# Performance work log

Measured on AMD Instinct MI355X. Metric: run time of the kernel, lower is better.

The kernel has to match this reference:

```python
import jax, jax.numpy as jnp
import numpy as np

N = 1024
INTER_CH = 10      # C(4,2) + (8-4)
HIDDEN_CH = 32
OUT_CH = 1
THRESH = 4
TOP_K = 8
INTERACT = 4


def setup_inputs() -> dict:
    key = jax.random.key(0)
    k1, k2, k3, k4, k5 = jax.random.split(key, 5)
    x = jax.random.normal(k1, (16, N, N), dtype=jnp.float32)
    is_active_flags = jnp.ones((16,), dtype=bool)
    # 1x1 conv params (stored as dense matrices; kernel_size=1)
    w1 = jax.random.normal(k2, (HIDDEN_CH, INTER_CH), dtype=jnp.float32) / np.sqrt(INTER_CH)
    b1 = jax.random.normal(k3, (HIDDEN_CH, 1, 1), dtype=jnp.float32) * 0.01
    w2 = jax.random.normal(k4, (OUT_CH, HIDDEN_CH), dtype=jnp.float32) / np.sqrt(HIDDEN_CH)
    b2 = jax.random.normal(k5, (OUT_CH, 1, 1), dtype=jnp.float32) * 0.01
    return {"x": x, "is_active_flags": is_active_flags, "w1": w1, "b1": b1, "w2": w2, "b2": b2}


def reference(x, is_active_flags, w1, b1, w2, b2):
    gate_active = jnp.sum(is_active_flags) >= THRESH

    def _active_path(operand):
        inputs, mask = operand                       # (16, n, n), (16,)
        _, slogdet = jnp.linalg.slogdet(inputs)      # (16,)
        scores = jnp.where(mask, slogdet, -jnp.inf)
        _, indices = jax.lax.top_k(scores, TOP_K)
        top_x = inputs[indices]                      # (8, n, n)
        top_interact_x = top_x[:INTERACT]            # (4, n, n)
        next_preserve_x = top_x[INTERACT:]           # (4, n, n)
        idx1, idx2 = jnp.triu_indices(INTERACT, k=1)  # 6 pairs
        pairs = jnp.matmul(top_interact_x[idx1], top_interact_x[idx2])  # (6, n, n)
        concat = jnp.concatenate([pairs, next_preserve_x], axis=0)      # (10, n, n)
        hidden = jnp.einsum('oc,chw->ohw', w1, concat) + b1             # 1x1 conv
        out = jnp.einsum('oc,chw->ohw', w2, hidden) + b2                # 1x1 conv
        return (out, jnp.array(True))

    def _inactive_path(operand):
        inputs, _ = operand
        _, n, m = inputs.shape
        return (jnp.zeros((OUT_CH, n, m), dtype=jnp.float32), jnp.array(False))

    out, out_active = jax.lax.cond(gate_active, _active_path, _inactive_path, (x, is_active_flags))
    return (out, out_active)
```

## Files before the change

kernel.cpp:

```cpp
#include <hip/hip_runtime.h>
#include <math.h>

#define N 1024
#define NN (N*N)

__device__ __forceinline__ void wave_argmax_kv(float& v, int& k) {
  #pragma unroll
  for (int off = 32; off > 0; off >>= 1) {
    float ov = __shfl_down(v, off);
    int   ok = __shfl_down(k, off);
    if (ov > v || (ov == v && ok < k)) { v = ov; k = ok; }
  }
}

__global__ void init_kernel(double* scores) {
  int t = threadIdx.x;
  if (t < 16) scores[t] = 0.0;
}

__global__ __launch_bounds__(256) void copy_kernel(const float4* __restrict__ src,
                                                   float4* __restrict__ dst) {
  int i = blockIdx.x * 256 + threadIdx.x;
  dst[i] = src[i];
}

__global__ __launch_bounds__(1024) void panel_kernel(float* __restrict__ lu,
                                                     int* __restrict__ ipiv,
                                                     double* __restrict__ scores,
                                                     int c0) {
  __shared__ __align__(16) float bufP[32];
  __shared__ float ujjS[32];
  __shared__ float redv[16];
  __shared__ int   redk[16];
  __shared__ int   posOf[1024];
  __shared__ int   lay[1024];
  const int m = blockIdx.x;
  float* A = lu + (size_t)m * NN;
  const int R = N - c0;
  const int tid = threadIdx.x;
  bool active = tid < R;
  float row[32];

  if (active) {
    const float4* g = (const float4*)(A + (size_t)(c0 + tid) * N + c0);
    #pragma unroll
    for (int q = 0; q < 8; ++q) {
      float4 v = g[q];
      row[4*q] = v.x; row[4*q+1] = v.y; row[4*q+2] = v.z; row[4*q+3] = v.w;
    }
  }
  posOf[tid] = tid;
  lay[tid]   = tid;
  __syncthreads();

  int worig;
  {
    float val = active ? fabsf(row[0]) : -1.0f;
    int key = (tid << 11) | tid;
    wave_argmax_kv(val, key);
    if ((tid & 63) == 0) { redv[tid >> 6] = val; redk[tid >> 6] = key; }
    __syncthreads();
    float bv = redv[0]; int bk = redk[0];
    #pragma unroll 1
    for (int w = 1; w < 16; ++w)
      if (redv[w] > bv || (redv[w] == bv && redk[w] < bk)) { bv = redv[w]; bk = redk[w]; }
    worig = bk & 0x7FF;
  }

  #pragma unroll
  for (int j = 0; j < 32; ++j) {
    if (tid == worig) {
      #pragma unroll
      for (int q = 0; q < 8; ++q)
        *(float4*)&bufP[4*q] = make_float4(row[4*q], row[4*q+1], row[4*q+2], row[4*q+3]);
      active = false;
    }
    if (tid == 0) {
      int p = posOf[worig];
      ipiv[m * 32 + j] = c0 + p;
      int a = lay[j];
      lay[j] = worig; lay[p] = a;
      posOf[worig] = j; posOf[a] = p;
    }
    __syncthreads();

    float u[32];
    #pragma unroll
    for (int q = 0; q < 8; ++q) {
      if (4*q + 3 >= j) {
        float4 v = *(const float4*)&bufP[4*q];
        u[4*q] = v.x; u[4*q+1] = v.y; u[4*q+2] = v.z; u[4*q+3] = v.w;
      }
    }
    if (tid == 0) ujjS[j] = u[j];
    const float rujj = 1.0f / u[j];

    float l = 0.0f;
    if (active) { l = row[j] * rujj; row[j] = l; }

    float val = -1.0f; int key = 0x7fffffff;
    if (j < 31) {
      if (active) {
        float v = row[j+1] - l * u[j+1];
        row[j+1] = v;
        #pragma unroll
        for (int jj = j + 2; jj < 32; ++jj) row[jj] -= l * u[jj];
        int mypos = posOf[tid];
        val = fabsf(v); key = (mypos << 11) | tid;
      }
      wave_argmax_kv(val, key);
      if ((tid & 63) == 0) { redv[tid >> 6] = val; redk[tid >> 6] = key; }
    }
    __syncthreads();
    if (j < 31) {
      float bv = redv[0]; int bk = redk[0];
      #pragma unroll 1
      for (int w = 1; w < 16; ++w)
        if (redv[w] > bv || (redv[w] == bv && redk[w] < bk)) { bv = redv[w]; bk = redk[w]; }
      worig = bk & 0x7FF;
    }
  }

  if (tid < R) {
    int fp = posOf[tid];
    float4* g = (float4*)(A + (size_t)(c0 + fp) * N + c0);
    #pragma unroll
    for (int q = 0; q < 8; ++q)
      g[q] = make_float4(row[4*q], row[4*q+1], row[4*q+2], row[4*q+3]);
  }
  if (tid == 0) {
    double logsum = 0.0;
    #pragma unroll 1
    for (int j = 0; j < 32; ++j) logsum += log(fabs((double)ujjS[j]));
    atomicAdd(&scores[m], logsum);
  }
}

__global__ __launch_bounds__(256) void ptrsm_kernel(float* __restrict__ lu,
                                                    const int* __restrict__ ipiv,
                                                    int c0, int ncs) {
  const int m  = blockIdx.x / ncs;
  const int cs = blockIdx.x % ncs;
  const int s0 = c0 + 32 + cs * 256;
  const int tid = threadIdx.x;
  const int col = s0 + tid;
  const bool ac = col < N;
  float* A = lu + (size_t)m * NN;
  const int R = N - c0;
  __shared__ int   rowAt[1024];
  __shared__ float L11s[32][33];
  __shared__ int   dDst[48];
  __shared__ int   dSrc[48];
  __shared__ int   dcount;

  for (int r = tid; r < R; r += 256) rowAt[r] = c0 + r;
  if (tid == 0) dcount = 0;
  for (int idx = tid; idx < 1024; idx += 256) {
    int i = idx >> 5, k = idx & 31;
    L11s[i][k] = A[(size_t)(c0 + i) * N + c0 + k];
  }
  __syncthreads();
  if (tid == 0) {
    #pragma unroll 1
    for (int j = 0; j < 32; ++j) {
      int p = ipiv[m * 32 + j];
      if (p != c0 + j) { int t = rowAt[j]; rowAt[j] = rowAt[p - c0]; rowAt[p - c0] = t; }
    }
  }
  __syncthreads();
  for (int r = 32 + tid; r < R; r += 256) {
    if (rowAt[r] != c0 + r) {
      int i = atomicAdd(&dcount, 1);
      dDst[i] = c0 + r; dSrc[i] = rowAt[r];
    }
  }
  __syncthreads();
  const int nd = dcount;

  float pay[32];
  #pragma unroll
  for (int i = 0; i < 32; ++i)
    if (i < nd && ac) pay[i] = A[(size_t)dSrc[i] * N + col];
  float u[32];
  #pragma unroll
  for (int i = 0; i < 32; ++i)
    if (ac) u[i] = A[(size_t)rowAt[i] * N + col];

  #pragma unroll
  for (int i = 1; i < 32; ++i) {
    float a = u[i];
    #pragma unroll
    for (int k = 0; k < 32; ++k)
      if (k < i) a -= L11s[i][k] * u[k];
    u[i] = a;
  }

  #pragma unroll
  for (int i = 0; i < 32; ++i)
    if (i < nd && ac) A[(size_t)dDst[i] * N + col] = pay[i];
  #pragma unroll
  for (int i = 0; i < 32; ++i)
    if (ac) A[(size_t)(c0 + i) * N + col] = u[i];
}

__global__ __launch_bounds__(256) void update_kernel(float* __restrict__ lu,
                                                     int c0, int nrt, int ncs) {
  const int per = nrt * ncs;
  const int m  = blockIdx.x / per;
  const int t  = blockIdx.x % per;
  const int rt = t / ncs, cs = t % ncs;
  const int r0 = c0 + 32 + rt * 64;
  const int s0 = c0 + 32 + cs * 256;
  const int tid = threadIdx.x;
  float* A = lu + (size_t)m * NN;
  __shared__ float Lts[32][68];
  __shared__ float Us[32][260];
  for (int idx = tid; idx < 2048; idx += 256) {
    int r = idx >> 5, k = idx & 31;
    Lts[k][r] = (r0 + r < N) ? A[(size_t)(r0 + r) * N + c0 + k] : 0.0f;
  }
  for (int idx = tid; idx < 8192; idx += 256) {
    int k = idx >> 8, c = idx & 255;
    Us[k][c] = (s0 + c < N) ? A[(size_t)(c0 + k) * N + s0 + c] : 0.0f;
  }
  __syncthreads();
  const int tx = tid & 63;
  const int ty = tid >> 6;
  float4 acc[16];
  #pragma unroll
  for (int e = 0; e < 16; ++e) acc[e] = make_float4(0.f, 0.f, 0.f, 0.f);
  #pragma unroll 4
  for (int k = 0; k < 32; ++k) {
    float4 b  = *(const float4*)&Us[k][tx * 4];
    float4 a0 = *(const float4*)&Lts[k][ty * 16 + 0];
    float4 a1 = *(const float4*)&Lts[k][ty * 16 + 4];
    float4 a2 = *(const float4*)&Lts[k][ty * 16 + 8];
    float4 a3 = *(const float4*)&Lts[k][ty * 16 + 12];
    acc[0].x  += a0.x*b.x; acc[0].y  += a0.x*b.y; acc[0].z  += a0.x*b.z; acc[0].w  += a0.x*b.w;
    acc[1].x  += a0.y*b.x; acc[1].y  += a0.y*b.y; acc[1].z  += a0.y*b.z; acc[1].w  += a0.y*b.w;
    acc[2].x  += a0.z*b.x; acc[2].y  += a0.z*b.y; acc[2].z  += a0.z*b.z; acc[2].w  += a0.z*b.w;
    acc[3].x  += a0.w*b.x; acc[3].y  += a0.w*b.y; acc[3].z  += a0.w*b.z; acc[3].w  += a0.w*b.w;
    acc[4].x  += a1.x*b.x; acc[4].y  += a1.x*b.y; acc[4].z  += a1.x*b.z; acc[4].w  += a1.x*b.w;
    acc[5].x  += a1.y*b.x; acc[5].y  += a1.y*b.y; acc[5].z  += a1.y*b.z; acc[5].w  += a1.y*b.w;
    acc[6].x  += a1.z*b.x; acc[6].y  += a1.z*b.y; acc[6].z  += a1.z*b.z; acc[6].w  += a1.z*b.w;
    acc[7].x  += a1.w*b.x; acc[7].y  += a1.w*b.y; acc[7].z  += a1.w*b.z; acc[7].w  += a1.w*b.w;
    acc[8].x  += a2.x*b.x; acc[8].y  += a2.x*b.y; acc[8].z  += a2.x*b.z; acc[8].w  += a2.x*b.w;
    acc[9].x  += a2.y*b.x; acc[9].y  += a2.y*b.y; acc[9].z  += a2.y*b.z; acc[9].w  += a2.y*b.w;
    acc[10].x += a2.z*b.x; acc[10].y += a2.z*b.y; acc[10].z += a2.z*b.z; acc[10].w += a2.z*b.w;
    acc[11].x += a2.w*b.x; acc[11].y += a2.w*b.y; acc[11].z += a2.w*b.z; acc[11].w += a2.w*b.w;
    acc[12].x += a3.x*b.x; acc[12].y += a3.x*b.y; acc[12].z += a3.x*b.z; acc[12].w += a3.x*b.w;
    acc[13].x += a3.y*b.x; acc[13].y += a3.y*b.y; acc[13].z += a3.y*b.z; acc[13].w += a3.y*b.w;
    acc[14].x += a3.z*b.x; acc[14].y += a3.z*b.y; acc[14].z += a3.z*b.z; acc[14].w += a3.z*b.w;
    acc[15].x += a3.w*b.x; acc[15].y += a3.w*b.y; acc[15].z += a3.w*b.z; acc[15].w += a3.w*b.w;
  }
  const bool colok = (s0 + tx * 4) < N;
  #pragma unroll
  for (int e = 0; e < 16; ++e) {
    int r = r0 + ty * 16 + e;
    if (r < N && colok) {
      float4* p = (float4*)&A[(size_t)r * N + s0 + tx * 4];
      float4 v = *p;
      v.x -= acc[e].x; v.y -= acc[e].y; v.z -= acc[e].z; v.w -= acc[e].w;
      *p = v;
    }
  }
}

__global__ void select_kernel(const void* __restrict__ flagsraw, const double* __restrict__ scores,
                              const float* __restrict__ w1, const float* __restrict__ b1,
                              const float* __restrict__ w2, const float* __restrict__ b2,
                              int* __restrict__ topidx, float* __restrict__ misc,
                              float* __restrict__ out_tail) {
  if (threadIdx.x != 0 || blockIdx.x != 0) return;
  const unsigned char* fb = (const unsigned char*)flagsraw;
  bool nonbin = false, off4 = false;
  for (int i = 0; i < 16; ++i) {
    if (fb[i] > 1) nonbin = true;
    if ((i & 3) && fb[i]) off4 = true;
  }
  int f[16]; int nact = 0;
  for (int i = 0; i < 16; ++i) {
    int v;
    if (nonbin)      v = (((const float*)flagsraw)[i] != 0.0f);
    else if (off4)   v = (fb[i] != 0);
    else             v = (((const int*)flagsraw)[i] != 0);
    f[i] = v; nact += v;
  }
  int gate = (nact >= 4) ? 1 : 0;
  double sc[16];
  for (int i = 0; i < 16; ++i) sc[i] = f[i] ? scores[i] : -1.0e300;
  bool used[16] = {};
  for (int k = 0; k < 8; ++k) {
    int bi = -1; double bv = 0.0;
    for (int i = 0; i < 16; ++i)
      if (!used[i] && (bi < 0 || sc[i] > bv)) { bv = sc[i]; bi = i; }
    used[bi] = true;
    topidx[k] = bi;
  }
  for (int cC = 0; cC < 10; ++cC) {
    float s = 0.0f;
    for (int h = 0; h < 32; ++h) s += w2[h] * w1[h * 10 + cC];
    misc[cC] = s;
  }
  float be = 0.0f;
  for (int h = 0; h < 32; ++h) be += w2[h] * b1[h];
  be += b2[0];
  misc[10] = be;
  ((int*)misc)[12] = gate;
  *out_tail = gate ? 1.0f : 0.0f;
}

__global__ __launch_bounds__(256) void build_m_kernel(const float* __restrict__ x,
                                                      const int* __restrict__ topidx,
                                                      const float* __restrict__ misc,
                                                      float* __restrict__ M) {
  int i = blockIdx.x * 256 + threadIdx.x;
  const float4* T1 = (const float4*)(x + (size_t)topidx[1] * NN);
  const float4* T2 = (const float4*)(x + (size_t)topidx[2] * NN);
  const float4* T3 = (const float4*)(x + (size_t)topidx[3] * NN);
  float w0 = misc[0], w1_ = misc[1], w2_ = misc[2], w3_ = misc[3], w4_ = misc[4], w5_ = misc[5];
  float4 t1 = T1[i], t2 = T2[i], t3 = T3[i];
  float4 m0, m1, m2;
  m0.x = w0 * t1.x + w1_ * t2.x + w2_ * t3.x;
  m0.y = w0 * t1.y + w1_ * t2.y + w2_ * t3.y;
  m0.z = w0 * t1.z + w1_ * t2.z + w2_ * t3.z;
  m0.w = w0 * t1.w + w1_ * t2.w + w2_ * t3.w;
  m1.x = w3_ * t2.x + w4_ * t3.x;
  m1.y = w3_ * t2.y + w4_ * t3.y;
  m1.z = w3_ * t2.z + w4_ * t3.z;
  m1.w = w3_ * t2.w + w4_ * t3.w;
  m2.x = w5_ * t3.x;  m2.y = w5_ * t3.y;  m2.z = w5_ * t3.z;  m2.w = w5_ * t3.w;
  ((float4*)M)[i] = m0;
  ((float4*)(M + NN))[i] = m1;
  ((float4*)(M + 2 * (size_t)NN))[i] = m2;
}

__global__ __launch_bounds__(256) void final_gemm_kernel(const float* __restrict__ x,
                                                         const float* __restrict__ M,
                                                         const int* __restrict__ topidx,
                                                         float* __restrict__ P) {
  const int chunk = blockIdx.x >> 8;
  const int t  = blockIdx.x & 255;
  const int tr = t >> 4, tc = t & 15;
  const int mi  = chunk >> 1;
  const int k0b = (chunk & 1) << 9;
  const float* A = x + (size_t)topidx[mi] * NN;
  const float* B = M + (size_t)mi * NN;
  __shared__ float As[32][68];
  __shared__ float Bs[32][68];
  const int ty = threadIdx.x >> 4, tx = threadIdx.x & 15;
  float acc[4][4] = {};
  for (int k0 = k0b; k0 < k0b + 512; k0 += 32) {
    for (int idx = threadIdx.x; idx < 2048; idx += 256) {
      int r = idx >> 5, k = idx & 31;
      As[k][r] = A[(size_t)(tr * 64 + r) * N + k0 + k];
    }
    for (int idx = threadIdx.x; idx < 2048; idx += 256) {
      int k = idx >> 6, cc = idx & 63;
      Bs[k][cc] = B[(size_t)(k0 + k) * N + tc * 64 + cc];
    }
    __syncthreads();
    #pragma unroll 8
    for (int k = 0; k < 32; ++k) {
      float4 a = *(const float4*)&As[k][ty * 4];
      float4 b = *(const float4*)&Bs[k][tx * 4];
      acc[0][0] += a.x * b.x; acc[0][1] += a.x * b.y; acc[0][2] += a.x * b.z; acc[0][3] += a.x * b.w;
      acc[1][0] += a.y * b.x; acc[1][1] += a.y * b.y; acc[1][2] += a.y * b.z; acc[1][3] += a.y * b.w;
      acc[2][0] += a.z * b.x; acc[2][1] += a.z * b.y; acc[2][2] += a.z * b.z; acc[2][3] += a.z * b.w;
      acc[3][0] += a.w * b.x; acc[3][1] += a.w * b.y; acc[3][2] += a.w * b.z; acc[3][3] += a.w * b.w;
    }
    __syncthreads();
  }
  float* Pc = P + (size_t)chunk * NN;
  #pragma unroll
  for (int i = 0; i < 4; ++i) {
    size_t r = (size_t)(tr * 64 + ty * 4 + i);
    float4 v = make_float4(acc[i][0], acc[i][1], acc[i][2], acc[i][3]);
    *(float4*)&Pc[r * N + tc * 64 + tx * 4] = v;
  }
}

__global__ __launch_bounds__(256) void reduce_out_kernel(const float* __restrict__ x,
                                                         const float* __restrict__ P,
                                                         const int* __restrict__ topidx,
                                                         const float* __restrict__ misc,
                                                         float* __restrict__ out) {
  int i = blockIdx.x * 256 + threadIdx.x;
  int gate = ((const int*)misc)[12];
  float4* o = (float4*)out;
  if (!gate) { o[i] = make_float4(0.f, 0.f, 0.f, 0.f); return; }
  float w6 = misc[6], w7 = misc[7], w8 = misc[8], w9 = misc[9], be = misc[10];
  float4 p0 = ((const float4*)(x + (size_t)topidx[4] * NN))[i];
  float4 p1 = ((const float4*)(x + (size_t)topidx[5] * NN))[i];
  float4 p2 = ((const float4*)(x + (size_t)topidx[6] * NN))[i];
  float4 p3 = ((const float4*)(x + (size_t)topidx[7] * NN))[i];
  float4 r;
  r.x = be + w6 * p0.x + w7 * p1.x + w8 * p2.x + w9 * p3.x;
  r.y = be + w6 * p0.y + w7 * p1.y + w8 * p2.y + w9 * p3.y;
  r.z = be + w6 * p0.z + w7 * p1.z + w8 * p2.z + w9 * p3.z;
  r.w = be + w6 * p0.w + w7 * p1.w + w8 * p2.w + w9 * p3.w;
  #pragma unroll
  for (int cN = 0; cN < 6; ++cN) {
    float4 q = ((const float4*)(P + (size_t)cN * NN))[i];
    r.x += q.x; r.y += q.y; r.z += q.z; r.w += q.w;
  }
  o[i] = r;
}

extern "C" void kernel_launch(void* const* d_in, const int* in_sizes, int n_in,
                              void* d_out, int out_size, void* d_ws, size_t ws_size,
                              hipStream_t stream) {
  const float* x  = (const float*)d_in[0];
  const void*  fl = d_in[1];
  const float* w1 = (const float*)d_in[2];
  const float* b1 = (const float*)d_in[3];
  const float* w2 = (const float*)d_in[4];
  const float* b2 = (const float*)d_in[5];
  float* out = (float*)d_out;

  char* ws = (char*)d_ws;
  float* LU = (float*)ws;
  float* Mm = (float*)ws;
  float* P  = (float*)(ws + (size_t)12 * 1024 * 1024);
  size_t tail = (size_t)16 * NN * sizeof(float);
  double* scores = (double*)(ws + tail);
  int*    ipiv   = (int*)(ws + tail + 256);
  int*    topidx = (int*)(ws + tail + 256 + 2304);
  float*  misc   = (float*)(ws + tail + 256 + 2304 + 256);

  init_kernel<<<1, 64, 0, stream>>>(scores);
  copy_kernel<<<16384, 256, 0, stream>>>((const float4*)x, (float4*)LU);

  for (int c0 = 0; c0 < N; c0 += 32) {
    panel_kernel<<<16, 1024, 0, stream>>>(LU, ipiv, scores, c0);
    int tcols = N - c0 - 32;
    if (tcols > 0) {
      int ncs = (tcols + 255) / 256;
      ptrsm_kernel<<<16 * ncs, 256, 0, stream>>>(LU, ipiv, c0, ncs);
      int nrt = (tcols + 63) / 64;
      update_kernel<<<16 * nrt * ncs, 256, 0, stream>>>(LU, c0, nrt, ncs);
    }
  }

  select_kernel<<<1, 64, 0, stream>>>(fl, scores, w1, b1, w2, b2, topidx, misc, out + NN);
  build_m_kernel<<<1024, 256, 0, stream>>>(x, topidx, misc, Mm);
  final_gemm_kernel<<<1536, 256, 0, stream>>>(x, Mm, topidx, P);
  reduce_out_kernel<<<1024, 256, 0, stream>>>(x, P, topidx, misc, out);
}
```

Measured before the change: 5.151 ms.

## Rewrite LU panel factorization as single-wavefront kernel with LDS-resident panel

The panel kernel now runs one 64-lane wavefront per matrix instead of 1024 threads. The whole 32-column panel is held in shared memory with a padded stride, pivot rows are swapped in place, and each pivot search is a single wave shuffle reduction, so the cross-wave __syncthreads reductions and the posOf/lay bookkeeping go away. The cost is that each lane now processes up to 16 rows serially per column step, all through shared-memory traffic. Only 16 blocks are launched, so parallelism on the panel step drops sharply.

```diff
diff --git a/kernel.cpp b/kernel.cpp
--- a/kernel.cpp
+++ b/kernel.cpp
@@ -3,15 +3,7 @@
 
 #define N 1024
 #define NN (N*N)
-
-__device__ __forceinline__ void wave_argmax_kv(float& v, int& k) {
-  #pragma unroll
-  for (int off = 32; off > 0; off >>= 1) {
-    float ov = __shfl_down(v, off);
-    int   ok = __shfl_down(k, off);
-    if (ov > v || (ov == v && ok < k)) { v = ov; k = ok; }
-  }
-}
+#define PST 36
 
 __global__ void init_kernel(double* scores) {
   int t = threadIdx.x;
@@ -24,116 +16,109 @@
   dst[i] = src[i];
 }
 
-__global__ __launch_bounds__(1024) void panel_kernel(float* __restrict__ lu,
-                                                     int* __restrict__ ipiv,
-                                                     double* __restrict__ scores,
-                                                     int c0) {
-  __shared__ __align__(16) float bufP[32];
+__global__ __launch_bounds__(64, 1) void panel_kernel(float* __restrict__ lu,
+                                                      int* __restrict__ ipiv,
+                                                      double* __restrict__ scores,
+                                                      int c0) {
+  __shared__ __align__(16) float sh[1024 * PST];
   __shared__ float ujjS[32];
-  __shared__ float redv[16];
-  __shared__ int   redk[16];
-  __shared__ int   posOf[1024];
-  __shared__ int   lay[1024];
   const int m = blockIdx.x;
   float* A = lu + (size_t)m * NN;
   const int R = N - c0;
-  const int tid = threadIdx.x;
-  bool active = tid < R;
-  float row[32];
-
-  if (active) {
-    const float4* g = (const float4*)(A + (size_t)(c0 + tid) * N + c0);
+  const int lane = threadIdx.x;
+
+  for (int r = lane; r < R; r += 64) {
+    const float4* g = (const float4*)(A + (size_t)(c0 + r) * N + c0);
+    float* d = &sh[r * PST];
     #pragma unroll
-    for (int q = 0; q < 8; ++q) {
-      float4 v = g[q];
-      row[4*q] = v.x; row[4*q+1] = v.y; row[4*q+2] = v.z; row[4*q+3] = v.w;
-    }
-  }
-  posOf[tid] = tid;
-  lay[tid]   = tid;
+    for (int q = 0; q < 8; ++q) *(float4*)&d[4 * q] = g[q];
+  }
   __syncthreads();
 
-  int worig;
+  int pcur;
   {
-    float val = active ? fabsf(row[0]) : -1.0f;
-    int key = (tid << 11) | tid;
-    wave_argmax_kv(val, key);
-    if ((tid & 63) == 0) { redv[tid >> 6] = val; redk[tid >> 6] = key; }
+    float bval = -1.0f; int brow = 0x7fffffff;
+    for (int r = lane; r < R; r += 64) {
+      float v = fabsf(sh[r * PST]);
+      if (v > bval) { bval = v; brow = r; }
+    }
+    #pragma unroll
+    for (int mask = 32; mask; mask >>= 1) {
+      float ov = __shfl_xor(bval, mask);
+      int   orr = __shfl_xor(brow, mask);
+      if (ov > bval || (ov == bval && orr < brow)) { bval = ov; brow = orr; }
+    }
+    pcur = brow;
+  }
+
+  #pragma unroll
+  for (int j = 0; j < 32; ++j) {
+    if (pcur != j && lane < 8) {
+      float4 a = *(float4*)&sh[j * PST + 4 * lane];
+      float4 b = *(float4*)&sh[pcur * PST + 4 * lane];
+      *(float4*)&sh[j * PST + 4 * lane] = b;
+      *(float4*)&sh[pcur * PST + 4 * lane] = a;
+    }
+    if (lane == 0) ipiv[m * 32 + j] = c0 + pcur;
     __syncthreads();
-    float bv = redv[0]; int bk = redk[0];
-    #pragma unroll 1
-    for (int w = 1; w < 16; ++w)
-      if (redv[w] > bv || (redv[w] == bv && redk[w] < bk)) { bv = redv[w]; bk = redk[w]; }
-    worig = bk & 0x7FF;
-  }
-
-  #pragma unroll
-  for (int j = 0; j < 32; ++j) {
-    if (tid == worig) {
-      #pragma unroll
-      for (int q = 0; q < 8; ++q)
-        *(float4*)&bufP[4*q] = make_float4(row[4*q], row[4*q+1], row[4*q+2], row[4*q+3]);
-      active = false;
-    }
-    if (tid == 0) {
-      int p = posOf[worig];
-      ipiv[m * 32 + j] = c0 + p;
-      int a = lay[j];
-      lay[j] = worig; lay[p] = a;
-      posOf[worig] = j; posOf[a] = p;
-    }
-    __syncthreads();
-
-    float u[32];
-    #pragma unroll
-    for (int q = 0; q < 8; ++q) {
-      if (4*q + 3 >= j) {
-        float4 v = *(const float4*)&bufP[4*q];
-        u[4*q] = v.x; u[4*q+1] = v.y; u[4*q+2] = v.z; u[4*q+3] = v.w;
-      }
-    }
-    if (tid == 0) ujjS[j] = u[j];
-    const float rujj = 1.0f / u[j];
-
-    float l = 0.0f;
-    if (active) { l = row[j] * rujj; row[j] = l; }
-
-    float val = -1.0f; int key = 0x7fffffff;
-    if (j < 31) {
-      if (active) {
-        float v = row[j+1] - l * u[j+1];
-        row[j+1] = v;
-        #pragma unroll
-        for (int jj = j + 2; jj < 32; ++jj) row[jj] -= l * u[jj];
-        int mypos = posOf[tid];
-        val = fabsf(v); key = (mypos << 11) | tid;
-      }
-      wave_argmax_kv(val, key);
-      if ((tid & 63) == 0) { redv[tid >> 6] = val; redk[tid >> 6] = key; }
-    }
-    __syncthreads();
-    if (j < 31) {
-      float bv = redv[0]; int bk = redk[0];
-      #pragma unroll 1
-      for (int w = 1; w < 16; ++w)
-        if (redv[w] > bv || (redv[w] == bv && redk[w] < bk)) { bv = redv[w]; bk = redk[w]; }
-      worig = bk & 0x7FF;
-    }
-  }
-
-  if (tid < R) {
-    int fp = posOf[tid];
-    float4* g = (float4*)(A + (size_t)(c0 + fp) * N + c0);
+
+    const float ujj = sh[j * PST + j];
+    if (lane == 0) ujjS[j] = ujj;
+    const float rujj = 1.0f / ujj;
+
+    float4 u4[8];
     #pragma unroll
     for (int q = 0; q < 8; ++q)
-      g[q] = make_float4(row[4*q], row[4*q+1], row[4*q+2], row[4*q+3]);
-  }
-  if (tid == 0) {
-    double logsum = 0.0;
-    #pragma unroll 1
-    for (int j = 0; j < 32; ++j) logsum += log(fabs((double)ujjS[j]));
-    atomicAdd(&scores[m], logsum);
-  }
+      if (4 * q + 3 >= j) u4[q] = *(const float4*)&sh[j * PST + 4 * q];
+
+    float bval = -1.0f; int brow = 0x7fffffff;
+    for (int r = lane; r < R; r += 64) {
+      if (r <= j) continue;
+      float* rp = &sh[r * PST];
+      float l = 0.0f;
+      float nv = 0.0f;
+      #pragma unroll
+      for (int q = 0; q < 8; ++q) {
+        if (4 * q + 3 < j) continue;
+        float4 v = *(float4*)&rp[4 * q];
+        #pragma unroll
+        for (int e = 0; e < 4; ++e) {
+          const int c = 4 * q + e;
+          float* pv = (&v.x) + e;
+          const float uu = (&u4[q].x)[e];
+          if (c == j)      { l = (*pv) * rujj; *pv = l; }
+          else if (c > j)  { *pv -= l * uu; if (c == j + 1) nv = *pv; }
+        }
+        *(float4*)&rp[4 * q] = v;
+      }
+      if (j < 31) {
+        float av = fabsf(nv);
+        if (av > bval) { bval = av; brow = r; }
+      }
+    }
+    if (j < 31) {
+      #pragma unroll
+      for (int mask = 32; mask; mask >>= 1) {
+        float ov = __shfl_xor(bval, mask);
+        int   orr = __shfl_xor(brow, mask);
+        if (ov > bval || (ov == bval && orr < brow)) { bval = ov; brow = orr; }
+      }
+      pcur = brow;
+    }
+    __syncthreads();
+  }
+
+  for (int r = lane; r < R; r += 64) {
+    float4* g = (float4*)(A + (size_t)(c0 + r) * N + c0);
+    const float* s = &sh[r * PST];
+    #pragma unroll
+    for (int q = 0; q < 8; ++q) g[q] = *(const float4*)&s[4 * q];
+  }
+  double lg = 0.0;
+  if (lane < 32) lg = log(fabs((double)ujjS[lane]));
+  #pragma unroll
+  for (int mask = 32; mask; mask >>= 1) lg += __shfl_xor(lg, mask);
+  if (lane == 0) atomicAdd(&scores[m], lg);
 }
 
 __global__ __launch_bounds__(256) void ptrsm_kernel(float* __restrict__ lu,
@@ -432,7 +417,7 @@
   copy_kernel<<<16384, 256, 0, stream>>>((const float4*)x, (float4*)LU);
 
   for (int c0 = 0; c0 < N; c0 += 32) {
-    panel_kernel<<<16, 1024, 0, stream>>>(LU, ipiv, scores, c0);
+    panel_kernel<<<16, 64, 0, stream>>>(LU, ipiv, scores, c0);
     int tcols = N - c0 - 32;
     if (tcols > 0) {
       int ncs = (tcols + 255) / 256;
```

Result: faster. 5.038 ms (-2.2%).
